# Kernel optimization log

Hardware: AMD Instinct MI355X
Metric: run time of the kernel (lower is better)

## Reference

```python
import jax, jax.numpy as jnp
import numpy as np

C = 512
CQ = C // 8
BN_EPS = 1e-5


def setup_inputs() -> dict:
    key = jax.random.key(0)
    ks = jax.random.split(key, 12)
    s = 0.02
    return {
        "x": jax.random.normal(ks[0], (4, C, 64, 64), dtype=jnp.float32),
        "qw": jax.random.normal(ks[1], (CQ, C), dtype=jnp.float32) * s,
        "qb": jnp.zeros((CQ,), dtype=jnp.float32),
        "kw": jax.random.normal(ks[2], (CQ, C), dtype=jnp.float32) * s,
        "kb": jnp.zeros((CQ,), dtype=jnp.float32),
        "vw": jax.random.normal(ks[3], (C, C), dtype=jnp.float32) * s,
        "vb": jnp.zeros((C,), dtype=jnp.float32),
        "gamma": jnp.zeros((1,), dtype=jnp.float32),
        "beta": jnp.zeros((1,), dtype=jnp.float32),
        "fw": jax.random.normal(ks[4], (C, 2 * C), dtype=jnp.float32) * s,
        "fb": jnp.zeros((C,), dtype=jnp.float32),
        "bn_w": jnp.ones((C,), dtype=jnp.float32),
        "bn_b": jnp.zeros((C,), dtype=jnp.float32),
    }


def reference(x, qw, qb, kw, kb, vw, vb, gamma, beta, fw, fb, bn_w, bn_b):
    b, c, h, w = x.shape
    n = h * w
    xf = x.reshape(b, c, n)  # [b, c, n]

    # ----- position attention -----
    q = jnp.einsum('oc,bcn->bon', qw, xf) + qb[None, :, None]  # [b, cq, n]
    k = jnp.einsum('oc,bcn->bon', kw, xf) + kb[None, :, None]
    v = jnp.einsum('oc,bcn->bon', vw, xf) + vb[None, :, None]  # [b, c, n]
    # scores[i, j] = q_i . k_j, softmax over j
    scores = jnp.einsum('bci,bcj->bij', q, k)  # [b, n, n]
    att = jax.nn.softmax(scores, axis=-1)
    pos = jnp.einsum('bcj,bij->bci', v, att)  # [b, c, n]
    pos_out = (gamma[0] * pos + xf).reshape(b, c, h, w)

    # ----- channel attention -----
    energy = jnp.einsum('bin,bjn->bij', xf, xf)  # [b, c, c]
    catt = jax.nn.softmax(energy, axis=-1)
    chan = jnp.einsum('bij,bjn->bin', catt, xf)
    chan_out = (beta[0] * chan + xf).reshape(b, c, h, w)

    # ----- fusion: 1x1 conv + BN (batch stats, training mode) + ReLU -----
    cat = jnp.concatenate([pos_out, chan_out], axis=1)  # [b, 2c, h, w]
    y = jnp.einsum('oc,bchw->bohw', fw, cat) + fb[None, :, None, None]
    mean = jnp.mean(y, axis=(0, 2, 3), keepdims=True)
    var = jnp.var(y, axis=(0, 2, 3), keepdims=True)
    yn = (y - mean) * jax.lax.rsqrt(var + BN_EPS)
    out = jax.nn.relu(yn * bn_w[None, :, None, None] + bn_b[None, :, None, None])
    return out
```

## Files before the change

kernel.cpp:

```cpp
#include <hip/hip_runtime.h>
#include <stdint.h>

typedef unsigned short u16;
typedef __attribute__((ext_vector_type(8))) short bf16x8;
typedef __attribute__((ext_vector_type(4))) float f32x4;

#define DEVI static __device__ __forceinline__

DEVI u16 f2bf(float f){
  union { float f; uint32_t u; } c; c.f = f;
  uint32_t u = c.u;
  u += 0x7FFFu + ((u >> 16) & 1u);
  return (u16)(u >> 16);
}
DEVI float b2f(u16 h){
  union { uint32_t u; float f; } c; c.u = ((uint32_t)h) << 16;
  return c.f;
}

DEVI void gload16(const u16* g, u16* l){
  __builtin_amdgcn_global_load_lds(
      (const __attribute__((address_space(1))) unsigned int*)g,
      (__attribute__((address_space(3))) unsigned int*)l, 16, 0, 0);
}

DEVI bf16x8 ldsrd(const void* base, int byte){
  return *reinterpret_cast<const bf16x8*>((const char*)base + byte);
}

template<int BM,int BN,int FM,int FN,int BIAS,int EPI,int SWZ,int KSPLIT=1>
__global__ __launch_bounds__(256) void gemm_bt(
    const u16* __restrict__ A, long long strideA, int lda,
    const u16* __restrict__ B, long long strideB, int ldb,
    void* __restrict__ C, long long strideC, int ldc,
    const float* __restrict__ bias, int K,
    const float* __restrict__ cscale, const u16* __restrict__ xadd,
    long long strideX, int ldx)
{
  constexpr int BK  = 32;
  constexpr int WTM = FM*16, WTN = FN*16;
  static_assert(BM == 2*WTM && BN == 2*WTN, "2x2 wave layout");
  __shared__ u16 As[BM*BK];
  __shared__ u16 Bs[BN*BK];

  int bx = blockIdx.x, by = blockIdx.y, bz = blockIdx.z;
  if(SWZ){
    const int gx = gridDim.x, gy = gridDim.y;
    const int nwg = gx * gy * gridDim.z;
    const int orig = bx + gx * (by + gy * bz);
    const int q = nwg >> 3, r = nwg & 7;
    const int xcd = orig & 7, i = orig >> 3;
    const int wg = (xcd < r ? xcd*(q+1) : r*(q+1) + (xcd-r)*q) + i;
    bx = wg % gx;
    const int t = wg / gx;
    by = t % gy;
    bz = t / gy;
  }

  const int zz = bz;
  const int z  = (KSPLIT > 1) ? zz / KSPLIT : zz;
  const int ks = (KSPLIT > 1) ? zz % KSPLIT : 0;
  const u16* Ab = A + (long long)z * strideA + (long long)ks * K;
  const u16* Bb = B + (long long)z * strideB + (long long)ks * K;

  const int tid  = threadIdx.x;
  const int lane = tid & 63, wid = tid >> 6;
  const int wr = wid >> 1, wc = wid & 1;
  const long long bm0 = (long long)by * BM;
  const long long bn0 = (long long)bx * BN;

  const int srow  = lane >> 2;
  const int scol  = (((lane & 3) ^ ((lane >> 3) & 3))) * 8;
  const int wrow  = wid * 16 + srow;
  constexpr int TA = BM/64, TB = BN/64;

  const int fr  = lane & 15;
  const int sl8 = ((lane >> 4) ^ ((lane >> 1) & 3)) * 8;

  f32x4 acc[FM][FN] = {};

  for(int k0 = 0; k0 < K; k0 += BK){
    __syncthreads();
    #pragma unroll
    for(int t=0;t<TA;t++)
      gload16(&Ab[(bm0 + t*64 + wrow)*lda + k0 + scol],
              &As[(t*64 + wid*16)*BK]);
    #pragma unroll
    for(int t=0;t<TB;t++)
      gload16(&Bb[(bn0 + t*64 + wrow)*ldb + k0 + scol],
              &Bs[(t*64 + wid*16)*BK]);
    __syncthreads();

    bf16x8 af[FM], bg[FN];
    #pragma unroll
    for(int m=0;m<FM;m++)
      af[m] = *reinterpret_cast<const bf16x8*>(&As[(wr*WTM + m*16 + fr)*BK + sl8]);
    #pragma unroll
    for(int n=0;n<FN;n++)
      bg[n] = *reinterpret_cast<const bf16x8*>(&Bs[(wc*WTN + n*16 + fr)*BK + sl8]);
    #pragma unroll
    for(int m=0;m<FM;m++)
      #pragma unroll
      for(int n=0;n<FN;n++)
        acc[m][n] = __builtin_amdgcn_mfma_f32_16x16x32_bf16(af[m], bg[n], acc[m][n], 0, 0, 0);
  }

  const int lr = (lane >> 4) * 4, lc = lane & 15;
  const float g = (EPI == 3) ? cscale[0] : 0.f;
  #pragma unroll
  for(int m=0;m<FM;m++){
    #pragma unroll
    for(int n=0;n<FN;n++){
      #pragma unroll
      for(int r=0;r<4;r++){
        long long row = bm0 + wr*WTM + m*16 + lr + r;
        long long col = bn0 + wc*WTN + n*16 + lc;
        float v = acc[m][n][r];
        if(BIAS == 1) v += bias[(int)row];
        if(BIAS == 2) v += bias[(int)col];
        long long idx = row * (long long)ldc + col;
        if(EPI == 0){
          ((float*)C + (long long)zz*strideC)[idx] = v;
        } else if(EPI == 1){
          ((float*)C + (long long)zz*strideC)[idx] += v;
        } else if(EPI == 2){
          ((u16*)C + (long long)zz*strideC)[idx] = f2bf(v);
        } else {
          float xv = b2f(xadd[(long long)z*strideX + row*(long long)ldx + col]);
          ((u16*)C + (long long)zz*strideC)[idx] = f2bf(g * v + xv);
        }
      }
    }
  }
}

__global__ __launch_bounds__(512, 4) void flash_pos(
    const u16* __restrict__ qkT,
    const u16* __restrict__ vB,
    const u16* __restrict__ xfT,
    u16* __restrict__ pcT,
    const float* __restrict__ gamma)
{
  __shared__ u16 Ks[2][64*64];
  __shared__ u16 Vs[256*64];
  __shared__ u16 Ps[64*64];
  __shared__ float RS[2][4][32];

  int flat = blockIdx.x + 64*(blockIdx.y + 2*blockIdx.z);
  flat = (flat & 7)*64 + (flat >> 3);
  const int bx = flat & 63;
  const int ch = (flat >> 6) & 1;
  const int z  = flat >> 7;

  const int q0 = bx*64, c0 = ch*256;
  const int tid = threadIdx.x, lane = tid & 63, wid = tid >> 6;
  const int wr = wid >> 2, wc = wid & 3;
  const int fr = lane & 15, fq = lane >> 4;

  const u16* qkb = qkT + (long long)z*4096*128;
  const u16* vbb = vB  + (long long)z*512*4096;

  const int srow  = lane >> 3;
  const int sslot = (lane & 7) ^ srow;

  bf16x8 qa[2][2];
  #pragma unroll
  for(int m=0;m<2;m++)
    #pragma unroll
    for(int kk=0;kk<2;kk++)
      qa[m][kk] = *reinterpret_cast<const bf16x8*>(
          &qkb[(long long)(q0 + wr*32 + m*16 + fr)*128 + kk*32 + fq*8]);

  const u16* kp  = qkb + (long long)(wid*8 + srow)*128 + 64 + sslot*8;
  const u16* vp0 = vbb + (long long)(c0 + wid*8 + srow)*4096 + sslot*8;

  const int xm   = (fr & 7) << 4;
  const int koff = (wc*16 + fr)*128 + ((fq*16) ^ xm);
  const int pab  = (wr*32 + fr)*128 + ((fq*16) ^ xm);
  const int vfb  = (wc*64 + fr)*128 + ((fq*16) ^ xm);
  const int kdst = wid * 1024;
  const int key2 = (wc*16 + fr)*2;
  int pwo[4];
  #pragma unroll
  for(int r=0;r<4;r++){
    int qr = fq*4 + r;
    pwo[r] = qr*128 + (key2 ^ ((qr & 7) << 4));
  }

  gload16(kp, (u16*)((char*)Ks + kdst));
  kp += 64*128;
  gload16(vp0,            &Vs[(  0 + wid*8)*64]);
  gload16(vp0 +  64*4096, &Vs[( 64 + wid*8)*64]);
  gload16(vp0 + 128*4096, &Vs[(128 + wid*8)*64]);
  gload16(vp0 + 192*4096, &Vs[(192 + wid*8)*64]);
  vp0 += 64;
  __syncthreads();

  f32x4 acc[2][4] = {};
  float rsacc[2][4] = {};

  for(int t=0;t<64;t++){
    const int kbase = (t & 1) ? 8192 : 0;
    bf16x8 kb0 = ldsrd(Ks, kbase + koff);
    bf16x8 kb1 = ldsrd(Ks, kbase + (koff ^ 64));
    f32x4 s[2] = {};
    #pragma unroll
    for(int m=0;m<2;m++){
      s[m] = __builtin_amdgcn_mfma_f32_16x16x32_bf16(qa[m][0], kb0, s[m], 0, 0, 0);
      s[m] = __builtin_amdgcn_mfma_f32_16x16x32_bf16(qa[m][1], kb1, s[m], 0, 0, 0);
    }

    #pragma unroll
    for(int m=0;m<2;m++){
      float e0 = exp2f(s[m][0]), e1 = exp2f(s[m][1]);
      float e2 = exp2f(s[m][2]), e3 = exp2f(s[m][3]);
      rsacc[m][0] += e0; rsacc[m][1] += e1;
      rsacc[m][2] += e2; rsacc[m][3] += e3;
      uint32_t p01, p23;
      asm("v_cvt_pk_bf16_f32 %0, %1, %2" : "=v"(p01) : "v"(e0), "v"(e1));
      asm("v_cvt_pk_bf16_f32 %0, %1, %2" : "=v"(p23) : "v"(e2), "v"(e3));
      char* pbase = (char*)Ps + wr*4096 + m*2048;
      *(u16*)(pbase + pwo[0]) = (u16)p01;
      *(u16*)(pbase + pwo[1]) = (u16)(p01 >> 16);
      *(u16*)(pbase + pwo[2]) = (u16)p23;
      *(u16*)(pbase + pwo[3]) = (u16)(p23 >> 16);
    }
    __syncthreads();

    if(t+1 < 64){
      gload16(kp, (u16*)((char*)Ks + (kbase ^ 8192) + kdst));
      kp += 64*128;
    }

    bf16x8 pa00 = ldsrd(Ps, pab);
    bf16x8 pa01 = ldsrd(Ps, pab ^ 64);
    bf16x8 pa10 = ldsrd(Ps, (pab + 2048));
    bf16x8 pa11 = ldsrd(Ps, (pab + 2048) ^ 64);
    __builtin_amdgcn_s_setprio(1);
    #pragma unroll
    for(int n=0;n<4;n++){
      bf16x8 v0 = ldsrd(Vs, vfb + n*2048);
      bf16x8 v1 = ldsrd(Vs, (vfb + n*2048) ^ 64);
      acc[0][n] = __builtin_amdgcn_mfma_f32_16x16x32_bf16(pa00, v0, acc[0][n], 0, 0, 0);
      acc[0][n] = __builtin_amdgcn_mfma_f32_16x16x32_bf16(pa01, v1, acc[0][n], 0, 0, 0);
      acc[1][n] = __builtin_amdgcn_mfma_f32_16x16x32_bf16(pa10, v0, acc[1][n], 0, 0, 0);
      acc[1][n] = __builtin_amdgcn_mfma_f32_16x16x32_bf16(pa11, v1, acc[1][n], 0, 0, 0);
    }
    __builtin_amdgcn_s_setprio(0);
    __syncthreads();

    if(t+1 < 64){
      gload16(vp0,            &Vs[(  0 + wid*8)*64]);
      gload16(vp0 +  64*4096, &Vs[( 64 + wid*8)*64]);
      gload16(vp0 + 128*4096, &Vs[(128 + wid*8)*64]);
      gload16(vp0 + 192*4096, &Vs[(192 + wid*8)*64]);
      vp0 += 64;
    }
  }

  #pragma unroll
  for(int m=0;m<2;m++)
    #pragma unroll
    for(int r=0;r<4;r++){
      float v = rsacc[m][r];
      #pragma unroll
      for(int o=1;o<16;o<<=1) v += __shfl_xor(v, o);
      rsacc[m][r] = v;
    }
  if(fr == 0){
    #pragma unroll
    for(int m=0;m<2;m++)
      #pragma unroll
      for(int r=0;r<4;r++)
        RS[wr][wc][m*16 + fq*4 + r] = rsacc[m][r];
  }
  __syncthreads();

  const float g = gamma[0];
  #pragma unroll
  for(int m=0;m<2;m++){
    float inv[4];
    #pragma unroll
    for(int r=0;r<4;r++){
      int rloc = m*16 + fq*4 + r;
      inv[r] = g / (RS[wr][0][rloc] + RS[wr][1][rloc] +
                    RS[wr][2][rloc] + RS[wr][3][rloc]);
    }
    #pragma unroll
    for(int n=0;n<4;n++){
      #pragma unroll
      for(int r=0;r<4;r++){
        int qrow = q0 + wr*32 + m*16 + fq*4 + r;
        int c    = c0 + wc*64 + n*16 + fr;
        float xv = b2f(xfT[((long long)z*4096 + qrow)*512 + c]);
        pcT[((long long)z*4096 + qrow)*1024 + c] = f2bf(acc[m][n][r]*inv[r] + xv);
      }
    }
  }
}

__global__ __launch_bounds__(256) void softmax_sum4(const u16* __restrict__ part,
                                                    u16* __restrict__ catt)
{
  const int row = blockIdx.x;
  const int b = row >> 9, i = row & 511;
  const int t = threadIdx.x;
  const int lane = t & 63, wid = t >> 6;
  float v0 = 0.f, v1 = 0.f;
  #pragma unroll
  for(int sl=0;sl<4;sl++){
    uint32_t pr = *reinterpret_cast<const uint32_t*>(
        &part[(((long long)(b*4 + sl)*512 + i)*512) + 2*t]);
    v0 += b2f((u16)pr);
    v1 += b2f((u16)(pr >> 16));
  }
  float m = fmaxf(v0, v1);
  #pragma unroll
  for(int o=32;o;o>>=1) m = fmaxf(m, __shfl_xor(m, o));
  __shared__ float sred[4];
  if(lane == 0) sred[wid] = m;
  __syncthreads();
  m = fmaxf(fmaxf(sred[0], sred[1]), fmaxf(sred[2], sred[3]));
  float e0 = __expf(v0 - m), e1 = __expf(v1 - m);
  float s = e0 + e1;
  #pragma unroll
  for(int o=32;o;o>>=1) s += __shfl_xor(s, o);
  __syncthreads();
  if(lane == 0) sred[wid] = s;
  __syncthreads();
  s = sred[0] + sred[1] + sred[2] + sred[3];
  float inv = 1.0f / s;
  uint32_t pk = (uint32_t)f2bf(e0 * inv) | ((uint32_t)f2bf(e1 * inv) << 16);
  *reinterpret_cast<uint32_t*>(&catt[(long long)row * 512 + 2*t]) = pk;
}

__global__ __launch_bounds__(256) void prep_weights(
    const float* __restrict__ qw, const float* __restrict__ kw,
    const float* __restrict__ vw, const float* __restrict__ fw,
    const float* __restrict__ qb, const float* __restrict__ kb,
    u16* __restrict__ qkwb, u16* __restrict__ vwb, u16* __restrict__ fwb,
    float* __restrict__ qkb)
{
  const float LOG2E = 1.4426950408889634f;
  long long i = (long long)blockIdx.x*256 + threadIdx.x;
  const float* src; u16* dst; long long o; float sc = 1.f;
  if(i < 8192){        src = qw; dst = qkwb;          o = i; sc = LOG2E; }
  else if(i < 16384){  src = kw; dst = qkwb + 32768;  o = i - 8192; }
  else if(i < 81920){  src = vw; dst = vwb;           o = i - 16384; }
  else if(i < 212992){ src = fw; dst = fwb;           o = i - 81920; }
  else if(i < 213024){
    int t = (int)(i - 212992) * 4;
    #pragma unroll
    for(int j=0;j<4;j++) qkb[t+j] = (t+j < 64) ? qb[t+j]*LOG2E : kb[t+j-64];
    return;
  } else return;
  float4 v = reinterpret_cast<const float4*>(src)[o];
  ushort4 w;
  w.x = f2bf(v.x*sc); w.y = f2bf(v.y*sc); w.z = f2bf(v.z*sc); w.w = f2bf(v.w*sc);
  reinterpret_cast<ushort4*>(dst)[o] = w;
}

__global__ __launch_bounds__(256) void transpose_cast(
    const float* __restrict__ x, u16* __restrict__ xfb, u16* __restrict__ xfT)
{
  __shared__ float tile[32][33];
  const int b  = blockIdx.z;
  const int n0 = blockIdx.x * 32, c0 = blockIdx.y * 32;
  const int tx = threadIdx.x, ty = threadIdx.y;
  const float* xp = x + (long long)b * 512 * 4096;
  #pragma unroll
  for(int i=0;i<4;i++){
    int c = c0 + ty + i*8;
    float v = xp[(long long)c*4096 + n0 + tx];
    tile[ty + i*8][tx] = v;
    xfb[((long long)b*512 + c)*4096 + n0 + tx] = f2bf(v);
  }
  __syncthreads();
  #pragma unroll
  for(int i=0;i<4;i++){
    int n = n0 + ty + i*8;
    xfT[((long long)b*4096 + n)*512 + c0 + tx] = f2bf(tile[tx][ty + i*8]);
  }
}

__global__ __launch_bounds__(256) void bn_stats(const float* __restrict__ y,
                                                float* __restrict__ stat)
{
  const int o = blockIdx.x, t = threadIdx.x;
  const int lane = t & 63, wid = t >> 6;
  float s = 0.f, ss = 0.f;
  for(int b=0;b<4;b++){
    const float* p = y + ((long long)b*512 + o)*4096;
    for(int i=t;i<4096;i+=256){ float v = p[i]; s += v; ss += v*v; }
  }
  #pragma unroll
  for(int off=32;off;off>>=1){ s += __shfl_xor(s, off); ss += __shfl_xor(ss, off); }
  __shared__ float sred[8];
  if(lane == 0){ sred[wid] = s; sred[wid+4] = ss; }
  __syncthreads();
  if(t == 0){
    float S  = sred[0]+sred[1]+sred[2]+sred[3];
    float SS = sred[4]+sred[5]+sred[6]+sred[7];
    float mean = S * (1.f/16384.f);
    float var  = SS * (1.f/16384.f) - mean*mean;
    stat[o*2]   = mean;
    stat[o*2+1] = rsqrtf(var + 1e-5f);
  }
}

__global__ __launch_bounds__(256) void bn_apply(float* __restrict__ y,
    const float* __restrict__ stat, const float* __restrict__ w,
    const float* __restrict__ bb)
{
  long long i = (long long)blockIdx.x*256 + threadIdx.x;
  float4 v = reinterpret_cast<float4*>(y)[i];
  int o = (int)(((i*4) >> 12) & 511);
  float mean = stat[o*2], rstd = stat[o*2+1];
  float sc = w[o] * rstd;
  float sh = bb[o] - mean * sc;
  v.x = fmaxf(v.x*sc + sh, 0.f);
  v.y = fmaxf(v.y*sc + sh, 0.f);
  v.z = fmaxf(v.z*sc + sh, 0.f);
  v.w = fmaxf(v.w*sc + sh, 0.f);
  reinterpret_cast<float4*>(y)[i] = v;
}

extern "C" void kernel_launch(void* const* d_in, const int* in_sizes, int n_in,
                              void* d_out, int out_size, void* d_ws, size_t ws_size,
                              hipStream_t stream)
{
  const float* x     = (const float*)d_in[0];
  const float* qw    = (const float*)d_in[1];
  const float* qb    = (const float*)d_in[2];
  const float* kw    = (const float*)d_in[3];
  const float* kb    = (const float*)d_in[4];
  const float* vw    = (const float*)d_in[5];
  const float* vb    = (const float*)d_in[6];
  const float* gamma = (const float*)d_in[7];
  const float* beta  = (const float*)d_in[8];
  const float* fw    = (const float*)d_in[9];
  const float* fb    = (const float*)d_in[10];
  const float* bnw   = (const float*)d_in[11];
  const float* bnb   = (const float*)d_in[12];
  float* out = (float*)d_out;
  (void)in_sizes; (void)n_in; (void)out_size; (void)ws_size;

  char* base = (char*)d_ws;
  size_t off = 0;
  auto alloc = [&](size_t bytes)->char* {
    char* p = base + off;
    off += (bytes + 255) & ~(size_t)255;
    return p;
  };
  const long long NB = 4, Cc = 512, Nn = 4096;

  u16*   xfT  = (u16*)alloc((size_t)NB*Nn*Cc*2);
  u16*   xfb  = (u16*)alloc((size_t)NB*Cc*Nn*2);
  u16*   qkwb = (u16*)alloc((size_t)128*Cc*2);
  float* qkb  = (float*)alloc(128*4);
  u16*   vwb  = (u16*)alloc((size_t)Cc*Cc*2);
  u16*   fwb  = (u16*)alloc((size_t)Cc*2*Cc*2);
  u16*   qkT  = (u16*)alloc((size_t)NB*Nn*128*2);
  u16*   vB   = (u16*)alloc((size_t)NB*Cc*Nn*2);
  u16*   pcT  = (u16*)alloc((size_t)NB*Nn*1024*2);
  u16*   epart= (u16*)alloc((size_t)16*Cc*Cc*2);
  u16*   catt = (u16*)alloc((size_t)NB*Cc*Cc*2);
  float* stat = (float*)alloc((size_t)Cc*2*4);

  prep_weights<<<dim3(833), dim3(256), 0, stream>>>(qw, kw, vw, fw, qb, kb,
                                                    qkwb, vwb, fwb, qkb);
  transpose_cast<<<dim3(128,16,4), dim3(32,8), 0, stream>>>(x, xfb, xfT);

  gemm_bt<64,64,2,2,2,2,1><<<dim3(2,64,4), dim3(256), 0, stream>>>(
      xfT, Nn*Cc, 512, qkwb, 0, 512, qkT, Nn*128, 128, qkb, 512,
      nullptr, nullptr, 0, 0);
  gemm_bt<128,128,4,4,1,2,1><<<dim3(32,4,4), dim3(256), 0, stream>>>(
      vwb, 0, 512, xfT, Nn*Cc, 512, vB, Cc*Nn, 4096, vb, 512,
      nullptr, nullptr, 0, 0);

  gemm_bt<128,128,4,4,0,2,1,4><<<dim3(4,4,16), dim3(256), 0, stream>>>(
      xfb, Cc*Nn, 4096, xfb, Cc*Nn, 4096, epart, Cc*Cc, 512, nullptr, 1024,
      nullptr, nullptr, 0, 0);
  softmax_sum4<<<dim3(2048), dim3(256), 0, stream>>>(epart, catt);
  gemm_bt<128,128,4,4,0,3,1><<<dim3(4,32,4), dim3(256), 0, stream>>>(
      xfT, Nn*Cc, 512, catt, Cc*Cc, 512, pcT + 512, Nn*1024, 1024, nullptr, 512,
      beta, xfT, Nn*Cc, 512);

  flash_pos<<<dim3(64,2,4), dim3(512), 0, stream>>>(qkT, vB, xfT, pcT, gamma);

  gemm_bt<128,128,4,4,1,0,1><<<dim3(32,4,4), dim3(256), 0, stream>>>(
      fwb, 0, 1024, pcT, Nn*1024, 1024, out, Cc*Nn, 4096, fb, 1024,
      nullptr, nullptr, 0, 0);

  bn_stats<<<dim3(512), dim3(256), 0, stream>>>(out, stat);
  bn_apply<<<dim3(8192), dim3(256), 0, stream>>>(out, stat, bnw, bnb);
}
```

Before: 260.4 us.

## Fuse BN statistics into fusion GEMM epilogue, restructure flash_pos to 4 waves

The fusion GEMM now writes bf16 output and computes per-row partial sums and sums of squares in its epilogue. A tiny finalize kernel and a bf16-reading apply kernel replace the separate full-tensor stats pass. The fp32 intermediate round trip goes away, at the cost of bf16 rounding of pre-BN activations. flash_pos moves from 8 waves of 32 query rows to 4 waves covering all 64 rows, giving more MFMA work per wave and more register pressure. The QK projection GEMM tile is also widened to 64x128.

```diff
diff --git a/kernel.cpp b/kernel.cpp
--- a/kernel.cpp
+++ b/kernel.cpp
@@ -35,7 +35,7 @@
     void* __restrict__ C, long long strideC, int ldc,
     const float* __restrict__ bias, int K,
     const float* __restrict__ cscale, const u16* __restrict__ xadd,
-    long long strideX, int ldx)
+    long long strideX, int ldx, float* __restrict__ red)
 {
   constexpr int BK  = 32;
   constexpr int WTM = FM*16, WTN = FN*16;
@@ -106,6 +106,35 @@
   }
 
   const int lr = (lane >> 4) * 4, lc = lane & 15;
+
+  if(EPI == 7){
+    u16* Cp = (u16*)C + (long long)zz*strideC;
+    #pragma unroll
+    for(int m=0;m<FM;m++){
+      #pragma unroll
+      for(int r=0;r<4;r++){
+        long long row = bm0 + wr*WTM + m*16 + lr + r;
+        float bv = bias[(int)row];
+        float s = 0.f, ss = 0.f;
+        #pragma unroll
+        for(int n=0;n<FN;n++){
+          long long col = bn0 + wc*WTN + n*16 + lc;
+          float v = acc[m][n][r] + bv;
+          Cp[row*(long long)ldc + col] = f2bf(v);
+          s += v; ss += v*v;
+        }
+        #pragma unroll
+        for(int o=1;o<16;o<<=1){ s += __shfl_xor(s, o); ss += __shfl_xor(ss, o); }
+        if(lc == 0){
+          int slot = (z*gridDim.x + bx)*2 + wc;
+          red[(int)row*512 + slot*2]     = s;
+          red[(int)row*512 + slot*2 + 1] = ss;
+        }
+      }
+    }
+    return;
+  }
+
   const float g = (EPI == 3) ? cscale[0] : 0.f;
   #pragma unroll
   for(int m=0;m<FM;m++){
@@ -134,7 +163,7 @@
   }
 }
 
-__global__ __launch_bounds__(512, 4) void flash_pos(
+__global__ __launch_bounds__(256, 2) void flash_pos(
     const u16* __restrict__ qkT,
     const u16* __restrict__ vB,
     const u16* __restrict__ xfT,
@@ -144,7 +173,7 @@
   __shared__ u16 Ks[2][64*64];
   __shared__ u16 Vs[256*64];
   __shared__ u16 Ps[64*64];
-  __shared__ float RS[2][4][32];
+  __shared__ float RS[4][64];
 
   int flat = blockIdx.x + 64*(blockIdx.y + 2*blockIdx.z);
   flat = (flat & 7)*64 + (flat >> 3);
@@ -154,29 +183,29 @@
 
   const int q0 = bx*64, c0 = ch*256;
   const int tid = threadIdx.x, lane = tid & 63, wid = tid >> 6;
-  const int wr = wid >> 2, wc = wid & 3;
+  const int wc = wid;
   const int fr = lane & 15, fq = lane >> 4;
 
   const u16* qkb = qkT + (long long)z*4096*128;
   const u16* vbb = vB  + (long long)z*512*4096;
 
-  const int srow  = lane >> 3;
-  const int sslot = (lane & 7) ^ srow;
-
-  bf16x8 qa[2][2];
-  #pragma unroll
-  for(int m=0;m<2;m++)
+  const int srow  = tid >> 3;
+  const int sslot = (tid & 7) ^ (srow & 7);
+
+  bf16x8 qa[4][2];
+  #pragma unroll
+  for(int m=0;m<4;m++)
     #pragma unroll
     for(int kk=0;kk<2;kk++)
       qa[m][kk] = *reinterpret_cast<const bf16x8*>(
-          &qkb[(long long)(q0 + wr*32 + m*16 + fr)*128 + kk*32 + fq*8]);
-
-  const u16* kp  = qkb + (long long)(wid*8 + srow)*128 + 64 + sslot*8;
-  const u16* vp0 = vbb + (long long)(c0 + wid*8 + srow)*4096 + sslot*8;
+          &qkb[(long long)(q0 + m*16 + fr)*128 + kk*32 + fq*8]);
+
+  const u16* kp = qkb + (long long)srow*128 + 64 + sslot*8;
+  const u16* vp = vbb + (long long)(c0 + srow)*4096 + sslot*8;
 
   const int xm   = (fr & 7) << 4;
   const int koff = (wc*16 + fr)*128 + ((fq*16) ^ xm);
-  const int pab  = (wr*32 + fr)*128 + ((fq*16) ^ xm);
+  const int pab  = fr*128 + ((fq*16) ^ xm);
   const int vfb  = (wc*64 + fr)*128 + ((fq*16) ^ xm);
   const int kdst = wid * 1024;
   const int key2 = (wc*16 + fr)*2;
@@ -187,39 +216,38 @@
     pwo[r] = qr*128 + (key2 ^ ((qr & 7) << 4));
   }
 
-  gload16(kp, (u16*)((char*)Ks + kdst));
+  gload16(kp,          (u16*)((char*)Ks + kdst));
+  gload16(kp + 32*128, (u16*)((char*)Ks + 4096 + kdst));
   kp += 64*128;
-  gload16(vp0,            &Vs[(  0 + wid*8)*64]);
-  gload16(vp0 +  64*4096, &Vs[( 64 + wid*8)*64]);
-  gload16(vp0 + 128*4096, &Vs[(128 + wid*8)*64]);
-  gload16(vp0 + 192*4096, &Vs[(192 + wid*8)*64]);
-  vp0 += 64;
+  #pragma unroll
+  for(int cc=0;cc<8;cc++)
+    gload16(vp + (long long)cc*32*4096, &Vs[(cc*32 + wid*8)*64]);
+  vp += 64;
   __syncthreads();
 
-  f32x4 acc[2][4] = {};
-  float rsacc[2][4] = {};
+  f32x4 acc[4][4] = {};
+  float rs[4][4] = {};
 
   for(int t=0;t<64;t++){
     const int kbase = (t & 1) ? 8192 : 0;
     bf16x8 kb0 = ldsrd(Ks, kbase + koff);
     bf16x8 kb1 = ldsrd(Ks, kbase + (koff ^ 64));
-    f32x4 s[2] = {};
-    #pragma unroll
-    for(int m=0;m<2;m++){
+    f32x4 s[4] = {};
+    #pragma unroll
+    for(int m=0;m<4;m++){
       s[m] = __builtin_amdgcn_mfma_f32_16x16x32_bf16(qa[m][0], kb0, s[m], 0, 0, 0);
       s[m] = __builtin_amdgcn_mfma_f32_16x16x32_bf16(qa[m][1], kb1, s[m], 0, 0, 0);
     }
 
     #pragma unroll
-    for(int m=0;m<2;m++){
+    for(int m=0;m<4;m++){
       float e0 = exp2f(s[m][0]), e1 = exp2f(s[m][1]);
       float e2 = exp2f(s[m][2]), e3 = exp2f(s[m][3]);
-      rsacc[m][0] += e0; rsacc[m][1] += e1;
-      rsacc[m][2] += e2; rsacc[m][3] += e3;
+      rs[m][0] += e0; rs[m][1] += e1; rs[m][2] += e2; rs[m][3] += e3;
       uint32_t p01, p23;
       asm("v_cvt_pk_bf16_f32 %0, %1, %2" : "=v"(p01) : "v"(e0), "v"(e1));
       asm("v_cvt_pk_bf16_f32 %0, %1, %2" : "=v"(p23) : "v"(e2), "v"(e3));
-      char* pbase = (char*)Ps + wr*4096 + m*2048;
+      char* pbase = (char*)Ps + m*2048;
       *(u16*)(pbase + pwo[0]) = (u16)p01;
       *(u16*)(pbase + pwo[1]) = (u16)(p01 >> 16);
       *(u16*)(pbase + pwo[2]) = (u16)p23;
@@ -228,69 +256,69 @@
     __syncthreads();
 
     if(t+1 < 64){
-      gload16(kp, (u16*)((char*)Ks + (kbase ^ 8192) + kdst));
+      const int kb2 = kbase ^ 8192;
+      gload16(kp,          (u16*)((char*)Ks + kb2 + kdst));
+      gload16(kp + 32*128, (u16*)((char*)Ks + kb2 + 4096 + kdst));
       kp += 64*128;
     }
 
-    bf16x8 pa00 = ldsrd(Ps, pab);
-    bf16x8 pa01 = ldsrd(Ps, pab ^ 64);
-    bf16x8 pa10 = ldsrd(Ps, (pab + 2048));
-    bf16x8 pa11 = ldsrd(Ps, (pab + 2048) ^ 64);
     __builtin_amdgcn_s_setprio(1);
     #pragma unroll
-    for(int n=0;n<4;n++){
-      bf16x8 v0 = ldsrd(Vs, vfb + n*2048);
-      bf16x8 v1 = ldsrd(Vs, (vfb + n*2048) ^ 64);
-      acc[0][n] = __builtin_amdgcn_mfma_f32_16x16x32_bf16(pa00, v0, acc[0][n], 0, 0, 0);
-      acc[0][n] = __builtin_amdgcn_mfma_f32_16x16x32_bf16(pa01, v1, acc[0][n], 0, 0, 0);
-      acc[1][n] = __builtin_amdgcn_mfma_f32_16x16x32_bf16(pa10, v0, acc[1][n], 0, 0, 0);
-      acc[1][n] = __builtin_amdgcn_mfma_f32_16x16x32_bf16(pa11, v1, acc[1][n], 0, 0, 0);
+    for(int kk=0;kk<2;kk++){
+      bf16x8 pa[4];
+      #pragma unroll
+      for(int m=0;m<4;m++) pa[m] = ldsrd(Ps, (pab + m*2048) ^ (kk*64));
+      #pragma unroll
+      for(int n=0;n<4;n++){
+        bf16x8 v = ldsrd(Vs, (vfb + n*2048) ^ (kk*64));
+        #pragma unroll
+        for(int m=0;m<4;m++)
+          acc[m][n] = __builtin_amdgcn_mfma_f32_16x16x32_bf16(pa[m], v, acc[m][n], 0, 0, 0);
+      }
     }
     __builtin_amdgcn_s_setprio(0);
     __syncthreads();
 
     if(t+1 < 64){
-      gload16(vp0,            &Vs[(  0 + wid*8)*64]);
-      gload16(vp0 +  64*4096, &Vs[( 64 + wid*8)*64]);
-      gload16(vp0 + 128*4096, &Vs[(128 + wid*8)*64]);
-      gload16(vp0 + 192*4096, &Vs[(192 + wid*8)*64]);
-      vp0 += 64;
-    }
-  }
-
-  #pragma unroll
-  for(int m=0;m<2;m++)
+      #pragma unroll
+      for(int cc=0;cc<8;cc++)
+        gload16(vp + (long long)cc*32*4096, &Vs[(cc*32 + wid*8)*64]);
+      vp += 64;
+    }
+  }
+
+  #pragma unroll
+  for(int m=0;m<4;m++)
     #pragma unroll
     for(int r=0;r<4;r++){
-      float v = rsacc[m][r];
+      float v = rs[m][r];
       #pragma unroll
       for(int o=1;o<16;o<<=1) v += __shfl_xor(v, o);
-      rsacc[m][r] = v;
+      rs[m][r] = v;
     }
   if(fr == 0){
     #pragma unroll
-    for(int m=0;m<2;m++)
+    for(int m=0;m<4;m++)
       #pragma unroll
       for(int r=0;r<4;r++)
-        RS[wr][wc][m*16 + fq*4 + r] = rsacc[m][r];
+        RS[wc][m*16 + fq*4 + r] = rs[m][r];
   }
   __syncthreads();
 
   const float g = gamma[0];
   #pragma unroll
-  for(int m=0;m<2;m++){
+  for(int m=0;m<4;m++){
     float inv[4];
     #pragma unroll
     for(int r=0;r<4;r++){
-      int rloc = m*16 + fq*4 + r;
-      inv[r] = g / (RS[wr][0][rloc] + RS[wr][1][rloc] +
-                    RS[wr][2][rloc] + RS[wr][3][rloc]);
+      int q = m*16 + fq*4 + r;
+      inv[r] = g / (RS[0][q] + RS[1][q] + RS[2][q] + RS[3][q]);
     }
     #pragma unroll
     for(int n=0;n<4;n++){
       #pragma unroll
       for(int r=0;r<4;r++){
-        int qrow = q0 + wr*32 + m*16 + fq*4 + r;
+        int qrow = q0 + m*16 + fq*4 + r;
         int c    = c0 + wc*64 + n*16 + fr;
         float xv = b2f(xfT[((long long)z*4096 + qrow)*512 + c]);
         pcT[((long long)z*4096 + qrow)*1024 + c] = f2bf(acc[m][n][r]*inv[r] + xv);
@@ -383,46 +411,42 @@
   }
 }
 
-__global__ __launch_bounds__(256) void bn_stats(const float* __restrict__ y,
-                                                float* __restrict__ stat)
-{
-  const int o = blockIdx.x, t = threadIdx.x;
-  const int lane = t & 63, wid = t >> 6;
+__global__ __launch_bounds__(256) void bn_finalize(const float* __restrict__ red,
+                                                   float* __restrict__ stat)
+{
+  int ch = blockIdx.x*256 + threadIdx.x;
+  if(ch >= 512) return;
   float s = 0.f, ss = 0.f;
-  for(int b=0;b<4;b++){
-    const float* p = y + ((long long)b*512 + o)*4096;
-    for(int i=t;i<4096;i+=256){ float v = p[i]; s += v; ss += v*v; }
-  }
-  #pragma unroll
-  for(int off=32;off;off>>=1){ s += __shfl_xor(s, off); ss += __shfl_xor(ss, off); }
-  __shared__ float sred[8];
-  if(lane == 0){ sred[wid] = s; sred[wid+4] = ss; }
-  __syncthreads();
-  if(t == 0){
-    float S  = sred[0]+sred[1]+sred[2]+sred[3];
-    float SS = sred[4]+sred[5]+sred[6]+sred[7];
-    float mean = S * (1.f/16384.f);
-    float var  = SS * (1.f/16384.f) - mean*mean;
-    stat[o*2]   = mean;
-    stat[o*2+1] = rsqrtf(var + 1e-5f);
-  }
-}
-
-__global__ __launch_bounds__(256) void bn_apply(float* __restrict__ y,
+  for(int j=0;j<256;j++){
+    s  += red[ch*512 + j*2];
+    ss += red[ch*512 + j*2 + 1];
+  }
+  float mean = s * (1.f/16384.f);
+  float var  = ss * (1.f/16384.f) - mean*mean;
+  stat[ch*2]   = mean;
+  stat[ch*2+1] = rsqrtf(var + 1e-5f);
+}
+
+__global__ __launch_bounds__(256) void bn_apply_b(const u16* __restrict__ y,
     const float* __restrict__ stat, const float* __restrict__ w,
-    const float* __restrict__ bb)
+    const float* __restrict__ bb, float* __restrict__ out)
 {
   long long i = (long long)blockIdx.x*256 + threadIdx.x;
-  float4 v = reinterpret_cast<float4*>(y)[i];
-  int o = (int)(((i*4) >> 12) & 511);
-  float mean = stat[o*2], rstd = stat[o*2+1];
-  float sc = w[o] * rstd;
-  float sh = bb[o] - mean * sc;
-  v.x = fmaxf(v.x*sc + sh, 0.f);
-  v.y = fmaxf(v.y*sc + sh, 0.f);
-  v.z = fmaxf(v.z*sc + sh, 0.f);
-  v.w = fmaxf(v.w*sc + sh, 0.f);
-  reinterpret_cast<float4*>(y)[i] = v;
+  bf16x8 v = *reinterpret_cast<const bf16x8*>(&y[i*8]);
+  int o = (int)(((i*8) >> 12) & 511);
+  float sc = w[o] * stat[o*2+1];
+  float sh = bb[o] - stat[o*2] * sc;
+  float4 lo, hi;
+  lo.x = fmaxf(b2f((u16)v[0])*sc + sh, 0.f);
+  lo.y = fmaxf(b2f((u16)v[1])*sc + sh, 0.f);
+  lo.z = fmaxf(b2f((u16)v[2])*sc + sh, 0.f);
+  lo.w = fmaxf(b2f((u16)v[3])*sc + sh, 0.f);
+  hi.x = fmaxf(b2f((u16)v[4])*sc + sh, 0.f);
+  hi.y = fmaxf(b2f((u16)v[5])*sc + sh, 0.f);
+  hi.z = fmaxf(b2f((u16)v[6])*sc + sh, 0.f);
+  hi.w = fmaxf(b2f((u16)v[7])*sc + sh, 0.f);
+  *reinterpret_cast<float4*>(&out[i*8])     = lo;
+  *reinterpret_cast<float4*>(&out[i*8 + 4]) = hi;
 }
 
 extern "C" void kernel_launch(void* const* d_in, const int* in_sizes, int n_in,
@@ -455,43 +479,46 @@
   const long long NB = 4, Cc = 512, Nn = 4096;
 
   u16*   xfT  = (u16*)alloc((size_t)NB*Nn*Cc*2);
+  u16*   fwb  = (u16*)alloc((size_t)Cc*2*Cc*2);
+  char*  region = (char*)(base + off);
   u16*   xfb  = (u16*)alloc((size_t)NB*Cc*Nn*2);
   u16*   qkwb = (u16*)alloc((size_t)128*Cc*2);
   float* qkb  = (float*)alloc(128*4);
   u16*   vwb  = (u16*)alloc((size_t)Cc*Cc*2);
-  u16*   fwb  = (u16*)alloc((size_t)Cc*2*Cc*2);
   u16*   qkT  = (u16*)alloc((size_t)NB*Nn*128*2);
   u16*   vB   = (u16*)alloc((size_t)NB*Cc*Nn*2);
   u16*   pcT  = (u16*)alloc((size_t)NB*Nn*1024*2);
   u16*   epart= (u16*)alloc((size_t)16*Cc*Cc*2);
   u16*   catt = (u16*)alloc((size_t)NB*Cc*Cc*2);
   float* stat = (float*)alloc((size_t)Cc*2*4);
+  float* red  = (float*)alloc((size_t)Cc*256*2*4);
+  u16*   ybf16= (u16*)region;
 
   prep_weights<<<dim3(833), dim3(256), 0, stream>>>(qw, kw, vw, fw, qb, kb,
                                                     qkwb, vwb, fwb, qkb);
   transpose_cast<<<dim3(128,16,4), dim3(32,8), 0, stream>>>(x, xfb, xfT);
 
-  gemm_bt<64,64,2,2,2,2,1><<<dim3(2,64,4), dim3(256), 0, stream>>>(
+  gemm_bt<64,128,2,4,2,2,1><<<dim3(1,64,4), dim3(256), 0, stream>>>(
       xfT, Nn*Cc, 512, qkwb, 0, 512, qkT, Nn*128, 128, qkb, 512,
-      nullptr, nullptr, 0, 0);
+      nullptr, nullptr, 0, 0, nullptr);
   gemm_bt<128,128,4,4,1,2,1><<<dim3(32,4,4), dim3(256), 0, stream>>>(
       vwb, 0, 512, xfT, Nn*Cc, 512, vB, Cc*Nn, 4096, vb, 512,
-      nullptr, nullptr, 0, 0);
+      nullptr, nullptr, 0, 0, nullptr);
 
   gemm_bt<128,128,4,4,0,2,1,4><<<dim3(4,4,16), dim3(256), 0, stream>>>(
       xfb, Cc*Nn, 4096, xfb, Cc*Nn, 4096, epart, Cc*Cc, 512, nullptr, 1024,
-      nullptr, nullptr, 0, 0);
+      nullptr, nullptr, 0, 0, nullptr);
   softmax_sum4<<<dim3(2048), dim3(256), 0, stream>>>(epart, catt);
   gemm_bt<128,128,4,4,0,3,1><<<dim3(4,32,4), dim3(256), 0, stream>>>(
       xfT, Nn*Cc, 512, catt, Cc*Cc, 512, pcT + 512, Nn*1024, 1024, nullptr, 512,
-      beta, xfT, Nn*Cc, 512);
-
-  flash_pos<<<dim3(64,2,4), dim3(512), 0, stream>>>(qkT, vB, xfT, pcT, gamma);
-
-  gemm_bt<128,128,4,4,1,0,1><<<dim3(32,4,4), dim3(256), 0, stream>>>(
-      fwb, 0, 1024, pcT, Nn*1024, 1024, out, Cc*Nn, 4096, fb, 1024,
-      nullptr, nullptr, 0, 0);
-
-  bn_stats<<<dim3(512), dim3(256), 0, stream>>>(out, stat);
-  bn_apply<<<dim3(8192), dim3(256), 0, stream>>>(out, stat, bnw, bnb);
-}
+      beta, xfT, Nn*Cc, 512, nullptr);
+
+  flash_pos<<<dim3(64,2,4), dim3(256), 0, stream>>>(qkT, vB, xfT, pcT, gamma);
+
+  gemm_bt<128,128,4,4,1,7,1><<<dim3(32,4,4), dim3(256), 0, stream>>>(
+      fwb, 0, 1024, pcT, Nn*1024, 1024, ybf16, Cc*Nn, 4096, fb, 1024,
+      nullptr, nullptr, 0, 0, red);
+
+  bn_finalize<<<dim3(2), dim3(256), 0, stream>>>(red, stat);
+  bn_apply_b<<<dim3(4096), dim3(256), 0, stream>>>(ybf16, stat, bnw, bnb, out);
+}
```

Result: no change. 265.6 us (+2.0%).
